# Kernel optimization log

Hardware: AMD Instinct MI355X
Metric: run time of the kernel (lower is better)

## Reference

```python
import jax, jax.numpy as jnp
import numpy as np
from math import sqrt

HEADS = 16
D_MODEL = 1024
HEAD_DIM = D_MODEL // HEADS  # 64
B, SEQ = 2, 2048


def setup_inputs() -> dict:
    key = jax.random.key(0)
    ks = jax.random.split(key, 8)
    k = jax.random.normal(ks[0], (B, SEQ, D_MODEL), dtype=jnp.float32)
    q = jax.random.normal(ks[1], (B, SEQ, D_MODEL), dtype=jnp.float32)
    v = jax.random.normal(ks[2], (B, SEQ, D_MODEL), dtype=jnp.float32)
    # causal mask, broadcast over batch and heads; masked_fill where mask == 0
    mask = jnp.tril(jnp.ones((SEQ, SEQ), dtype=jnp.int32))[None, None, :, :]
    s = 1.0 / sqrt(HEAD_DIM)
    Wq = jax.random.normal(ks[3], (HEAD_DIM, HEAD_DIM), dtype=jnp.float32) * s
    Wk = jax.random.normal(ks[4], (HEAD_DIM, HEAD_DIM), dtype=jnp.float32) * s
    Wv = jax.random.normal(ks[5], (HEAD_DIM, HEAD_DIM), dtype=jnp.float32) * s
    Wo = jax.random.normal(ks[6], (D_MODEL, D_MODEL), dtype=jnp.float32) * (1.0 / sqrt(D_MODEL))
    bo = jax.random.normal(ks[7], (D_MODEL,), dtype=jnp.float32) * 0.01
    return {"key": k, "query": q, "value": v, "mask": mask,
            "Wq": Wq, "Wk": Wk, "Wv": Wv, "Wo": Wo, "bo": bo}


def reference(key, query, value, mask, Wq, Wk, Wv, Wo, bo):
    b, q_len, d = query.shape
    k_len = key.shape[1]
    hd = d // HEADS
    # reshape to [b, len, heads, head_dim]
    k = key.reshape(b, k_len, HEADS, hd)
    q = query.reshape(b, q_len, HEADS, hd)
    v = value.reshape(b, k_len, HEADS, hd)
    # per-head-dim Linear (weights shared across heads); torch Linear: y = x @ W.T
    k = jnp.einsum('bkhd,ed->bkhe', k, Wk)
    q = jnp.einsum('bqhd,ed->bqhe', q, Wq)
    v = jnp.einsum('bvhd,ed->bvhe', v, Wv)
    # full attention matrix [b, h, q, k]
    product = jnp.einsum('bqhd,bkhd->bhqk', q, k)
    # NOTE: original masks BEFORE scaling by 1/sqrt(head_dim)
    product = jnp.where(mask == 0, jnp.float32(-1e20), product)
    product = product / jnp.float32(sqrt(hd))
    score = jax.nn.softmax(product, axis=-1)
    out = jnp.einsum('bhqv,bvhd->bqhd', score, v).reshape(b, q_len, d)
    out = out @ Wo.T + bo
    return out
```

## Files before the change

### kernel.cpp

```cpp
#include <hip/hip_runtime.h>

typedef __bf16 bf16x8 __attribute__((ext_vector_type(8)));
typedef float  f32x4  __attribute__((ext_vector_type(4)));
typedef unsigned int uint32x4 __attribute__((ext_vector_type(4)));
typedef short  s16x4  __attribute__((ext_vector_type(4)));

#define MFMA16(a, b, c)  __builtin_amdgcn_mfma_f32_16x16x32_bf16((a), (b), (c), 0, 0, 0)
#define MFMAK16(a, b, c) __builtin_amdgcn_mfma_f32_16x16x16bf16_1k((a), (b), (c), 0, 0, 0)

constexpr int SEQ = 2048;
constexpr int DM  = 1024;
constexpr int NH  = 16;
constexpr int HD  = 64;
constexpr int BATCH = 2;


union Bf4 { __bf16 h[4]; s16x4 v; unsigned int u[2]; };

__device__ inline bf16x8 ld8_f32(const float* p) {
    f32x4 a = *(const f32x4*)p;
    f32x4 b = *(const f32x4*)(p + 4);
    bf16x8 r;
    r[0] = (__bf16)a[0]; r[1] = (__bf16)a[1]; r[2] = (__bf16)a[2]; r[3] = (__bf16)a[3];
    r[4] = (__bf16)b[0]; r[5] = (__bf16)b[1]; r[6] = (__bf16)b[2]; r[7] = (__bf16)b[3];
    return r;
}

__global__ __launch_bounds__(256)
void proj_kernel(const float* __restrict__ Xq, const float* __restrict__ Xk,
                 const float* __restrict__ Xv,
                 const float* __restrict__ Wq, const float* __restrict__ Wk,
                 const float* __restrict__ Wv,
                 __bf16* __restrict__ Qp, __bf16* __restrict__ Kp,
                 __bf16* __restrict__ Vp)
{
    const int tid  = threadIdx.x;
    const int w    = tid >> 6;
    const int lane = tid & 63;
    const int quad = lane >> 4;
    const int l16  = lane & 15;
    const int sblk = blockIdx.x;
    const int bh   = blockIdx.y;
    const int tz   = blockIdx.z;

    const float* X = (tz == 0) ? Xq : (tz == 1) ? Xk : Xv;
    const float* W = (tz == 0) ? Wq : (tz == 1) ? Wk : Wv;
    __bf16*      O = (tz == 0) ? Qp : (tz == 1) ? Kp : Vp;
    const float scale = (tz == 0) ? (0.125f * 1.44269504088896f) : 1.0f;

    const int b = bh >> 4, h = bh & 15;
    const int mrow = sblk * 64 + w * 16 + l16;

    const size_t xoff = (size_t)(b * SEQ + mrow) * DM + h * HD + quad * 8;
    bf16x8 a0 = ld8_f32(X + xoff);
    bf16x8 a1 = ld8_f32(X + xoff + 32);

    f32x4 acc[4];
    #pragma unroll
    for (int nt = 0; nt < 4; ++nt) {
        const size_t woff = (size_t)(nt * 16 + l16) * HD + quad * 8;
        bf16x8 b0 = ld8_f32(W + woff);
        bf16x8 b1 = ld8_f32(W + woff + 32);
        f32x4 c = {0.f, 0.f, 0.f, 0.f};
        c = MFMA16(a0, b0, c);
        c = MFMA16(a1, b1, c);
        acc[nt] = c;
    }

    __bf16* obase = O + (size_t)bh * SEQ * HD;
    #pragma unroll
    for (int nt = 0; nt < 4; ++nt) {
        #pragma unroll
        for (int r = 0; r < 4; ++r) {
            const int srow = sblk * 64 + w * 16 + quad * 4 + r;
            obase[(size_t)srow * HD + nt * 16 + l16] = (__bf16)(acc[nt][r] * scale);
        }
    }
}

__global__ __launch_bounds__(256, 2)
void attn_kernel(const __bf16* __restrict__ Qp, const __bf16* __restrict__ Kp,
                 const __bf16* __restrict__ Vp, __bf16* __restrict__ AO)
{
    __shared__ __align__(16) unsigned int K_lds[2][64 * 36];
    __shared__ __align__(16) unsigned int VT2[2][64 * 36];

    const int tid  = threadIdx.x;
    const int w    = tid >> 6;
    const int lane = tid & 63;
    const int quad = lane >> 4;
    const int l16  = lane & 15;
    const int pr   = blockIdx.x;
    const int bh   = blockIdx.y;

    const __bf16* Qb = Qp + (size_t)bh * SEQ * HD;
    const __bf16* Kb = Kp + (size_t)bh * SEQ * HD;
    const __bf16* Vb = Vp + (size_t)bh * SEQ * HD;

    Bf4 ones_a;
    #pragma unroll
    for (int i = 0; i < 4; ++i) ones_a.h[i] = (l16 == 0) ? (__bf16)1.0f : (__bf16)0.0f;

    const int krow = tid >> 3, kcol = tid & 7;
    const int jp = tid & 31, d0 = (tid >> 5) * 8;

    #pragma unroll
    for (int phase = 0; phase < 2; ++phase) {
        const int tile = (phase == 0) ? (31 - pr) : pr;
        const int q0   = tile * 64;
        const int nkc  = tile + 1;

        __syncthreads();

        const int qrow = q0 + w * 16 + l16;
        bf16x8 qa0 = *(const bf16x8*)(Qb + (size_t)qrow * HD + quad * 8);
        bf16x8 qa1 = *(const bf16x8*)(Qb + (size_t)qrow * HD + quad * 8 + 32);

        f32x4 accT[4];
        #pragma unroll
        for (int dm = 0; dm < 4; ++dm) { f32x4 z = {0.f,0.f,0.f,0.f}; accT[dm] = z; }
        f32x4 acc5 = {0.f, 0.f, 0.f, 0.f};

        uint32x4 kpre0 = *(const uint32x4*)(Kb + (size_t)krow * HD + kcol * 8);
        uint32x4 kpre1 = *(const uint32x4*)(Kb + (size_t)(krow + 32) * HD + kcol * 8);
        uint32x4 vlo   = *(const uint32x4*)(Vb + (size_t)(2 * jp) * HD + d0);
        uint32x4 vhi   = *(const uint32x4*)(Vb + (size_t)(2 * jp + 1) * HD + d0);

        for (int kc = 0; kc < nkc; ++kc) {
            const int buf = kc & 1;
            *(uint32x4*)&K_lds[buf][krow * 36 + kcol * 4]        = kpre0;
            *(uint32x4*)&K_lds[buf][(krow + 32) * 36 + kcol * 4] = kpre1;
            #pragma unroll
            for (int i2 = 0; i2 < 4; ++i2) {
                const unsigned int va = vlo[i2], vb = vhi[i2];
                VT2[buf][(d0 + 2 * i2    ) * 36 + jp] = (va & 0xffffu) | (vb << 16);
                VT2[buf][(d0 + 2 * i2 + 1) * 36 + jp] = (va >> 16) | (vb & 0xffff0000u);
            }
            __syncthreads();

            if (kc + 1 < nkc) {
                const size_t o = (size_t)(kc + 1) * 64;
                kpre0 = *(const uint32x4*)(Kb + (o + krow) * HD + kcol * 8);
                kpre1 = *(const uint32x4*)(Kb + (o + krow + 32) * HD + kcol * 8);
                vlo   = *(const uint32x4*)(Vb + (o + 2 * jp) * HD + d0);
                vhi   = *(const uint32x4*)(Vb + (o + 2 * jp + 1) * HD + d0);
            }

            f32x4 st[4];
            #pragma unroll
            for (int nt = 0; nt < 4; ++nt) {
                const unsigned int* kb = &K_lds[buf][(nt * 16 + l16) * 36 + quad * 4];
                bf16x8 kb0 = *(const bf16x8*)(kb);
                bf16x8 kb1 = *(const bf16x8*)(kb + 16);
                f32x4 c = {0.f, 0.f, 0.f, 0.f};
                c = MFMA16(kb0, qa0, c);
                c = MFMA16(kb1, qa1, c);
                st[nt] = c;
            }
            if (kc == tile) {
                #pragma unroll
                for (int nt = 0; nt < 4; ++nt) {
                    #pragma unroll
                    for (int r = 0; r < 4; ++r) {
                        const int j = kc * 64 + nt * 16 + quad * 4 + r;
                        if (j > qrow) st[nt][r] = -1e30f;
                    }
                }
            }
            Bf4 pf[4];
            #pragma unroll
            for (int nt = 0; nt < 4; ++nt) {
                #pragma unroll
                for (int r = 0; r < 4; ++r) pf[nt].h[r] = (__bf16)exp2f(st[nt][r]);
            }
            #pragma unroll
            for (int nt = 0; nt < 4; ++nt) {
                #pragma unroll
                for (int dm = 0; dm < 4; ++dm) {
                    Bf4 va;
                    va.u[0] = VT2[buf][(dm * 16 + l16) * 36 + nt * 8 + quad * 2];
                    va.u[1] = VT2[buf][(dm * 16 + l16) * 36 + nt * 8 + quad * 2 + 1];
                    accT[dm] = MFMAK16(va.v, pf[nt].v, accT[dm]);
                }
                acc5 = MFMAK16(ones_a.v, pf[nt].v, acc5);
            }
        }

        const int b = bh >> 4, h = bh & 15;
        const float ls  = __shfl(acc5[0], l16, 64);
        const float inv = 1.0f / ls;
        #pragma unroll
        for (int dm = 0; dm < 4; ++dm) {
            Bf4 ov;
            #pragma unroll
            for (int r = 0; r < 4; ++r) ov.h[r] = (__bf16)(accT[dm][r] * inv);
            *(unsigned long long*)(AO + (size_t)(b * SEQ + qrow) * DM + h * HD
                                   + dm * 16 + quad * 4) =
                *(const unsigned long long*)&ov.u[0];
        }
    }
}

__global__ __launch_bounds__(256)
void wconv_kernel(const float* __restrict__ Wo, __bf16* __restrict__ Wb)
{
    const size_t i = ((size_t)blockIdx.x * 256 + threadIdx.x) * 8;
    *(bf16x8*)(Wb + i) = ld8_f32(Wo + i);
}

__global__ __launch_bounds__(256)
void ogemm_kernel(const __bf16* __restrict__ AO, const __bf16* __restrict__ Wb,
                  const float* __restrict__ bo, float* __restrict__ out)
{
    __shared__ __align__(16) unsigned int A_lds[2][64 * 36];
    __shared__ __align__(16) unsigned int B_lds[2][128 * 36];

    const int tid  = threadIdx.x;
    const int w    = tid >> 6;
    const int lane = tid & 63;
    const int quad = lane >> 4;
    const int l16  = lane & 15;
    const int m0   = blockIdx.x * 64;
    const int n0   = blockIdx.y * 128;

    const int row = tid >> 3, c = tid & 7;

    f32x4 acc[8];
    #pragma unroll
    for (int nt = 0; nt < 8; ++nt) { f32x4 z = {0.f,0.f,0.f,0.f}; acc[nt] = z; }

    uint32x4 apre[2], bpre[4];
    #pragma unroll
    for (int i = 0; i < 2; ++i)
        apre[i] = *(const uint32x4*)(AO + (size_t)(m0 + row + i * 32) * DM + c * 8);
    #pragma unroll
    for (int i = 0; i < 4; ++i)
        bpre[i] = *(const uint32x4*)(Wb + (size_t)(n0 + row + i * 32) * DM + c * 8);

    for (int kc = 0; kc < DM / 64; ++kc) {
        const int buf = kc & 1;
        #pragma unroll
        for (int i = 0; i < 2; ++i)
            *(uint32x4*)&A_lds[buf][(row + i * 32) * 36 + c * 4] = apre[i];
        #pragma unroll
        for (int i = 0; i < 4; ++i)
            *(uint32x4*)&B_lds[buf][(row + i * 32) * 36 + c * 4] = bpre[i];
        __syncthreads();

        if (kc + 1 < DM / 64) {
            const size_t o = (size_t)(kc + 1) * 64;
            #pragma unroll
            for (int i = 0; i < 2; ++i)
                apre[i] = *(const uint32x4*)(AO + (size_t)(m0 + row + i * 32) * DM + o + c * 8);
            #pragma unroll
            for (int i = 0; i < 4; ++i)
                bpre[i] = *(const uint32x4*)(Wb + (size_t)(n0 + row + i * 32) * DM + o + c * 8);
        }

        #pragma unroll
        for (int ks = 0; ks < 2; ++ks) {
            bf16x8 a = *(const bf16x8*)&A_lds[buf][(w * 16 + l16) * 36 + ks * 16 + quad * 4];
            #pragma unroll
            for (int nt = 0; nt < 8; ++nt) {
                bf16x8 bb = *(const bf16x8*)&B_lds[buf][(nt * 16 + l16) * 36 + ks * 16 + quad * 4];
                acc[nt] = MFMA16(a, bb, acc[nt]);
            }
        }
    }

    #pragma unroll
    for (int nt = 0; nt < 8; ++nt) {
        const int n = n0 + nt * 16 + l16;
        const float bof = bo[n];
        #pragma unroll
        for (int r = 0; r < 4; ++r) {
            const int m = m0 + w * 16 + quad * 4 + r;
            out[(size_t)m * DM + n] = acc[nt][r] + bof;
        }
    }
}

extern "C" void kernel_launch(void* const* d_in, const int* in_sizes, int n_in,
                              void* d_out, int out_size, void* d_ws, size_t ws_size,
                              hipStream_t stream)
{
    const float* key   = (const float*)d_in[0];
    const float* query = (const float*)d_in[1];
    const float* value = (const float*)d_in[2];
    const float* Wq = (const float*)d_in[4];
    const float* Wk = (const float*)d_in[5];
    const float* Wv = (const float*)d_in[6];
    const float* Wo = (const float*)d_in[7];
    const float* bo = (const float*)d_in[8];

    const size_t per = (size_t)BATCH * NH * SEQ * HD;
    __bf16* Qp = (__bf16*)d_ws;
    __bf16* Kp = Qp + per;
    __bf16* Vp = Kp + per;
    __bf16* AO = Vp + per;
    __bf16* Wb = Kp;

    proj_kernel<<<dim3(SEQ / 64, BATCH * NH, 3), 256, 0, stream>>>(
        query, key, value, Wq, Wk, Wv, Qp, Kp, Vp);
    attn_kernel<<<dim3(SEQ / 128, BATCH * NH), 256, 0, stream>>>(Qp, Kp, Vp, AO);
    wconv_kernel<<<dim3(DM * DM / (256 * 8)), 256, 0, stream>>>(Wo, Wb);
    ogemm_kernel<<<dim3(BATCH * SEQ / 64, DM / 128), 256, 0, stream>>>(
        AO, Wb, bo, (float*)d_out);
}
```

Before: 200.1 us.

## Store V transposed in projection and load K/V fragments directly in attention

The projection kernel now writes V in a transposed, key-permuted layout so the attention kernel can load MFMA operand fragments for K and V straight from global memory into registers. This removes the LDS staging buffers, the in-kernel V transpose and all __syncthreads in the attention loop. The cost is that each wave independently reloads the whole K/V tile from global/L2, roughly four times the previous global traffic, and the software prefetch of the next tile is gone, so load latency is less hidden.

```diff
diff --git a/kernel.cpp b/kernel.cpp
--- a/kernel.cpp
+++ b/kernel.cpp
@@ -15,7 +15,8 @@
 constexpr int BATCH = 2;
 
 
-union Bf4 { __bf16 h[4]; s16x4 v; unsigned int u[2]; };
+union Bf4 { __bf16 h[4]; s16x4 v; unsigned int u[2]; unsigned long long ull; };
+union Bf8 { __bf16 h[8]; bf16x8 b; s16x4 v[2]; uint32x4 q; };
 
 __device__ inline bf16x8 ld8_f32(const float* p) {
     f32x4 a = *(const f32x4*)p;
@@ -32,7 +33,7 @@
                  const float* __restrict__ Wq, const float* __restrict__ Wk,
                  const float* __restrict__ Wv,
                  __bf16* __restrict__ Qp, __bf16* __restrict__ Kp,
-                 __bf16* __restrict__ Vp)
+                 __bf16* __restrict__ VT)
 {
     const int tid  = threadIdx.x;
     const int w    = tid >> 6;
@@ -45,7 +46,6 @@
 
     const float* X = (tz == 0) ? Xq : (tz == 1) ? Xk : Xv;
     const float* W = (tz == 0) ? Wq : (tz == 1) ? Wk : Wv;
-    __bf16*      O = (tz == 0) ? Qp : (tz == 1) ? Kp : Vp;
     const float scale = (tz == 0) ? (0.125f * 1.44269504088896f) : 1.0f;
 
     const int b = bh >> 4, h = bh & 15;
@@ -67,24 +67,33 @@
         acc[nt] = c;
     }
 
-    __bf16* obase = O + (size_t)bh * SEQ * HD;
-    #pragma unroll
-    for (int nt = 0; nt < 4; ++nt) {
-        #pragma unroll
-        for (int r = 0; r < 4; ++r) {
-            const int srow = sblk * 64 + w * 16 + quad * 4 + r;
-            obase[(size_t)srow * HD + nt * 16 + l16] = (__bf16)(acc[nt][r] * scale);
+    if (tz < 2) {
+        __bf16* obase = ((tz == 0) ? Qp : Kp) + (size_t)bh * SEQ * HD;
+        #pragma unroll
+        for (int nt = 0; nt < 4; ++nt) {
+            #pragma unroll
+            for (int r = 0; r < 4; ++r) {
+                const int srow = sblk * 64 + w * 16 + quad * 4 + r;
+                obase[(size_t)srow * HD + nt * 16 + l16] = (__bf16)(acc[nt][r] * scale);
+            }
+        }
+    } else {
+        __bf16* vbase = VT + (size_t)bh * HD * SEQ;
+        #pragma unroll
+        for (int nt = 0; nt < 4; ++nt) {
+            Bf4 ov;
+            #pragma unroll
+            for (int r = 0; r < 4; ++r) ov.h[r] = (__bf16)acc[nt][r];
+            *(unsigned long long*)(vbase + (size_t)(nt * 16 + l16) * SEQ
+                                   + sblk * 64 + quad * 16 + w * 4) = ov.ull;
         }
     }
 }
 
 __global__ __launch_bounds__(256, 2)
 void attn_kernel(const __bf16* __restrict__ Qp, const __bf16* __restrict__ Kp,
-                 const __bf16* __restrict__ Vp, __bf16* __restrict__ AO)
-{
-    __shared__ __align__(16) unsigned int K_lds[2][64 * 36];
-    __shared__ __align__(16) unsigned int VT2[2][64 * 36];
-
+                 const __bf16* __restrict__ VT, __bf16* __restrict__ AO)
+{
     const int tid  = threadIdx.x;
     const int w    = tid >> 6;
     const int lane = tid & 63;
@@ -95,14 +104,11 @@
 
     const __bf16* Qb = Qp + (size_t)bh * SEQ * HD;
     const __bf16* Kb = Kp + (size_t)bh * SEQ * HD;
-    const __bf16* Vb = Vp + (size_t)bh * SEQ * HD;
+    const __bf16* Vt = VT + (size_t)bh * HD * SEQ;
 
     Bf4 ones_a;
     #pragma unroll
     for (int i = 0; i < 4; ++i) ones_a.h[i] = (l16 == 0) ? (__bf16)1.0f : (__bf16)0.0f;
-
-    const int krow = tid >> 3, kcol = tid & 7;
-    const int jp = tid & 31, d0 = (tid >> 5) * 8;
 
     #pragma unroll
     for (int phase = 0; phase < 2; ++phase) {
@@ -110,8 +116,6 @@
         const int q0   = tile * 64;
         const int nkc  = tile + 1;
 
-        __syncthreads();
-
         const int qrow = q0 + w * 16 + l16;
         bf16x8 qa0 = *(const bf16x8*)(Qb + (size_t)qrow * HD + quad * 8);
         bf16x8 qa1 = *(const bf16x8*)(Qb + (size_t)qrow * HD + quad * 8 + 32);
@@ -121,40 +125,27 @@
         for (int dm = 0; dm < 4; ++dm) { f32x4 z = {0.f,0.f,0.f,0.f}; accT[dm] = z; }
         f32x4 acc5 = {0.f, 0.f, 0.f, 0.f};
 
-        uint32x4 kpre0 = *(const uint32x4*)(Kb + (size_t)krow * HD + kcol * 8);
-        uint32x4 kpre1 = *(const uint32x4*)(Kb + (size_t)(krow + 32) * HD + kcol * 8);
-        uint32x4 vlo   = *(const uint32x4*)(Vb + (size_t)(2 * jp) * HD + d0);
-        uint32x4 vhi   = *(const uint32x4*)(Vb + (size_t)(2 * jp + 1) * HD + d0);
-
         for (int kc = 0; kc < nkc; ++kc) {
-            const int buf = kc & 1;
-            *(uint32x4*)&K_lds[buf][krow * 36 + kcol * 4]        = kpre0;
-            *(uint32x4*)&K_lds[buf][(krow + 32) * 36 + kcol * 4] = kpre1;
-            #pragma unroll
-            for (int i2 = 0; i2 < 4; ++i2) {
-                const unsigned int va = vlo[i2], vb = vhi[i2];
-                VT2[buf][(d0 + 2 * i2    ) * 36 + jp] = (va & 0xffffu) | (vb << 16);
-                VT2[buf][(d0 + 2 * i2 + 1) * 36 + jp] = (va >> 16) | (vb & 0xffff0000u);
-            }
-            __syncthreads();
-
-            if (kc + 1 < nkc) {
-                const size_t o = (size_t)(kc + 1) * 64;
-                kpre0 = *(const uint32x4*)(Kb + (o + krow) * HD + kcol * 8);
-                kpre1 = *(const uint32x4*)(Kb + (o + krow + 32) * HD + kcol * 8);
-                vlo   = *(const uint32x4*)(Vb + (o + 2 * jp) * HD + d0);
-                vhi   = *(const uint32x4*)(Vb + (o + 2 * jp + 1) * HD + d0);
-            }
-
+            bf16x8 kf0[4], kf1[4];
+            #pragma unroll
+            for (int nt = 0; nt < 4; ++nt) {
+                const __bf16* kp = Kb + (size_t)(kc * 64 + nt * 16 + l16) * HD + quad * 8;
+                kf0[nt] = *(const bf16x8*)(kp);
+                kf1[nt] = *(const bf16x8*)(kp + 32);
+            }
+            Bf8 vf[4][2];
+            #pragma unroll
+            for (int dm = 0; dm < 4; ++dm) {
+                const __bf16* vp = Vt + (size_t)(dm * 16 + l16) * SEQ + kc * 64 + quad * 16;
+                vf[dm][0].q = *(const uint32x4*)(vp);
+                vf[dm][1].q = *(const uint32x4*)(vp + 8);
+            }
             f32x4 st[4];
             #pragma unroll
             for (int nt = 0; nt < 4; ++nt) {
-                const unsigned int* kb = &K_lds[buf][(nt * 16 + l16) * 36 + quad * 4];
-                bf16x8 kb0 = *(const bf16x8*)(kb);
-                bf16x8 kb1 = *(const bf16x8*)(kb + 16);
                 f32x4 c = {0.f, 0.f, 0.f, 0.f};
-                c = MFMA16(kb0, qa0, c);
-                c = MFMA16(kb1, qa1, c);
+                c = MFMA16(kf0[nt], qa0, c);
+                c = MFMA16(kf1[nt], qa1, c);
                 st[nt] = c;
             }
             if (kc == tile) {
@@ -174,15 +165,14 @@
                 for (int r = 0; r < 4; ++r) pf[nt].h[r] = (__bf16)exp2f(st[nt][r]);
             }
             #pragma unroll
-            for (int nt = 0; nt < 4; ++nt) {
+            for (int a = 0; a < 2; ++a) {
                 #pragma unroll
                 for (int dm = 0; dm < 4; ++dm) {
-                    Bf4 va;
-                    va.u[0] = VT2[buf][(dm * 16 + l16) * 36 + nt * 8 + quad * 2];
-                    va.u[1] = VT2[buf][(dm * 16 + l16) * 36 + nt * 8 + quad * 2 + 1];
-                    accT[dm] = MFMAK16(va.v, pf[nt].v, accT[dm]);
+                    accT[dm] = MFMAK16(vf[dm][a].v[0], pf[2 * a].v,     accT[dm]);
+                    accT[dm] = MFMAK16(vf[dm][a].v[1], pf[2 * a + 1].v, accT[dm]);
                 }
-                acc5 = MFMAK16(ones_a.v, pf[nt].v, acc5);
+                acc5 = MFMAK16(ones_a.v, pf[2 * a].v,     acc5);
+                acc5 = MFMAK16(ones_a.v, pf[2 * a + 1].v, acc5);
             }
         }
 
@@ -195,8 +185,7 @@
             #pragma unroll
             for (int r = 0; r < 4; ++r) ov.h[r] = (__bf16)(accT[dm][r] * inv);
             *(unsigned long long*)(AO + (size_t)(b * SEQ + qrow) * DM + h * HD
-                                   + dm * 16 + quad * 4) =
-                *(const unsigned long long*)&ov.u[0];
+                                   + dm * 16 + quad * 4) = ov.ull;
         }
     }
 }
@@ -296,13 +285,13 @@
     const size_t per = (size_t)BATCH * NH * SEQ * HD;
     __bf16* Qp = (__bf16*)d_ws;
     __bf16* Kp = Qp + per;
-    __bf16* Vp = Kp + per;
-    __bf16* AO = Vp + per;
+    __bf16* VT = Kp + per;
+    __bf16* AO = VT + per;
     __bf16* Wb = Kp;
 
     proj_kernel<<<dim3(SEQ / 64, BATCH * NH, 3), 256, 0, stream>>>(
-        query, key, value, Wq, Wk, Wv, Qp, Kp, Vp);
-    attn_kernel<<<dim3(SEQ / 128, BATCH * NH), 256, 0, stream>>>(Qp, Kp, Vp, AO);
+        query, key, value, Wq, Wk, Wv, Qp, Kp, VT);
+    attn_kernel<<<dim3(SEQ / 128, BATCH * NH), 256, 0, stream>>>(Qp, Kp, VT, AO);
     wconv_kernel<<<dim3(DM * DM / (256 * 8)), 256, 0, stream>>>(Wo, Wb);
     ogemm_kernel<<<dim3(BATCH * SEQ / 64, DM / 128), 256, 0, stream>>>(
         AO, Wb, bo, (float*)d_out);
```

Result: slower. 281.9 us (+40.9%).
